# Kernel tuning notes

Measured on AMD Instinct MI355X. Metric: run time of the kernel, lower is better.

The kernel has to match this reference:

```python
import jax, jax.numpy as jnp
import numpy as np

EMBED_DIM = 1024
NUM_HEADS = 16
HEAD_DIM = EMBED_DIM // NUM_HEADS  # 64
QK_SCALE = 0.125  # head_dim ** -0.5, passed as qk_scale in __init__
B, LQ, LKV = 2, 2048, 2048


def setup_inputs() -> dict:
    key = jax.random.key(0)
    ks = jax.random.split(key, 7)
    std = 0.02
    return {
        "q": jax.random.normal(ks[0], (B, LQ, EMBED_DIM), dtype=jnp.float32),
        "k": jax.random.normal(ks[1], (B, LKV, EMBED_DIM), dtype=jnp.float32),
        "v": jax.random.normal(ks[2], (B, LKV, EMBED_DIM), dtype=jnp.float32),
        "Wq": jax.random.normal(ks[3], (EMBED_DIM, EMBED_DIM), dtype=jnp.float32) * std,
        "Wk": jax.random.normal(ks[4], (EMBED_DIM, EMBED_DIM), dtype=jnp.float32) * std,
        "Wv": jax.random.normal(ks[5], (EMBED_DIM, EMBED_DIM), dtype=jnp.float32) * std,
        "Wo": jax.random.normal(ks[6], (EMBED_DIM, EMBED_DIM), dtype=jnp.float32) * std,
    }


def _split_heads(x):
    # rearrange 'b l (c n) -> b n l c' with n = num_heads (heads are the INNER sub-dim)
    b, l, _ = x.shape
    return x.reshape(b, l, HEAD_DIM, NUM_HEADS).transpose(0, 3, 1, 2)  # (b, n, l, c)


def reference(q, k, v, Wq, Wk, Wv, Wo):
    b = q.shape[0]
    qh = _split_heads(q @ Wq)  # (b, n, lq, c)
    kh = _split_heads(k @ Wk)  # (b, n, lkv, c)
    vh = _split_heads(v @ Wv)  # (b, n, lkv, c)
    # attn = (q * qk_scale) @ k^T / sqrt(batch)
    scores = jnp.einsum('bnqc,bnkc->bnqk', qh * QK_SCALE, kh)
    scores = scores / jnp.sqrt(jnp.float32(b))
    attn = jax.nn.softmax(scores, axis=-1)
    out = jnp.einsum('bnqk,bnkc->bnqc', attn, vh)  # (b, n, lq, c)
    # merge heads back with the inverse of the (c n) split: b n l c -> b l (c n)
    out = out.transpose(0, 2, 3, 1).reshape(b, -1, HEAD_DIM * NUM_HEADS)
    return out @ Wo  # output projection (b, lq, embed_dim)
```

## Files before the change

### kernel.cpp

```cpp
#include <hip/hip_runtime.h>
#include <hip/hip_bf16.h>


typedef __attribute__((ext_vector_type(8))) short short8;
typedef __attribute__((ext_vector_type(4))) float f32x4;
typedef __attribute__((ext_vector_type(16))) float f32x16;
typedef __hip_bfloat16 bf16;

#define GLD16(g, l) __builtin_amdgcn_global_load_lds( \
    (const __attribute__((address_space(1))) void*)(g), \
    (__attribute__((address_space(3))) void*)(l), 16, 0, 0)

#define VMCNT(n) do { asm volatile("s_waitcnt vmcnt(" #n ")" ::: "memory"); \
                      __builtin_amdgcn_sched_barrier(0); } while (0)
#define BAR() do { __builtin_amdgcn_sched_barrier(0); __builtin_amdgcn_s_barrier(); \
                   __builtin_amdgcn_sched_barrier(0); } while (0)

__device__ __forceinline__ f32x4 mfma16(short8 a, short8 b, f32x4 c) {
  return __builtin_amdgcn_mfma_f32_16x16x32_bf16(a, b, c, 0, 0, 0);
}
__device__ __forceinline__ f32x16 mfma32(short8 a, short8 b, f32x16 c) {
  return __builtin_amdgcn_mfma_f32_32x32x16_bf16(a, b, c, 0, 0, 0);
}

union B8 { bf16 h[8]; int4 v; };
union B4 { bf16 h[4]; int2 v; };

#define QK_SCALE_TOT 0.08838834764831845f
#define SC2f (QK_SCALE_TOT * 1.4426950408889634f)

__device__ __forceinline__ float fexp2(float x) {
#if __has_builtin(__builtin_amdgcn_exp2f)
  return __builtin_amdgcn_exp2f(x);
#else
  return exp2f(x);
#endif
}

__device__ __forceinline__ int cvtpk(float lo, float hi_) {
  int r;
  asm("v_cvt_pk_bf16_f32 %0, %1, %2" : "=v"(r) : "v"(lo), "v"(hi_));
  return r;
}

#define ZV16 {0.f,0.f,0.f,0.f,0.f,0.f,0.f,0.f,0.f,0.f,0.f,0.f,0.f,0.f,0.f,0.f}

__global__ __launch_bounds__(256) void cast3_kernel(
    const float* __restrict__ q, const float* __restrict__ k,
    const float* __restrict__ v, bf16* __restrict__ out)
{
  const float* src = (blockIdx.y == 0) ? q : (blockIdx.y == 1) ? k : v;
  bf16* dst = out + (size_t)blockIdx.y * (4u << 20);
  size_t i = ((size_t)blockIdx.x * 256 + threadIdx.x) * 8;
  float4 a = *(const float4*)(src + i);
  float4 b = *(const float4*)(src + i + 4);
  B8 u;
  u.h[0] = __float2bfloat16(a.x); u.h[1] = __float2bfloat16(a.y);
  u.h[2] = __float2bfloat16(a.z); u.h[3] = __float2bfloat16(a.w);
  u.h[4] = __float2bfloat16(b.x); u.h[5] = __float2bfloat16(b.y);
  u.h[6] = __float2bfloat16(b.z); u.h[7] = __float2bfloat16(b.w);
  *(int4*)(dst + i) = u.v;
}

__global__ __launch_bounds__(256) void wtrans_kernel(
    const float* __restrict__ Wq, const float* __restrict__ Wk,
    const float* __restrict__ Wv, const float* __restrict__ Wo,
    bf16* __restrict__ dstbase)
{
  __shared__ bf16 ld[64][68];
  const int z = blockIdx.z;
  const float* src = (z == 0) ? Wq : (z == 1) ? Wk : (z == 2) ? Wv : Wo;
  bf16* dst = dstbase + (size_t)z * (1u << 20);
  const int k0 = blockIdx.x * 64, n0 = blockIdx.y * 64;
  const int t = threadIdx.x;
  const bool perm = (z == 3);
#pragma unroll
  for (int it = 0; it < 4; ++it) {
    int kk = it * 16 + (t >> 4);
    int K = k0 + kk;
    int j = perm ? ((K & 63) * 16 + (K >> 6)) : K;
    float4 vv = *(const float4*)(src + (size_t)j * 1024 + n0 + (t & 15) * 4);
    int c = (t & 15) * 4;
    ld[c + 0][kk] = __float2bfloat16(vv.x);
    ld[c + 1][kk] = __float2bfloat16(vv.y);
    ld[c + 2][kk] = __float2bfloat16(vv.z);
    ld[c + 3][kk] = __float2bfloat16(vv.w);
  }
  __syncthreads();
#pragma unroll
  for (int it = 0; it < 2; ++it) {
    int rr = it * 32 + (t >> 3), cc = (t & 7) * 8;
    B8 u;
#pragma unroll
    for (int e = 0; e < 8; ++e) u.h[e] = ld[rr][cc + e];
    *(int4*)(dst + (size_t)(n0 + rr) * 1024 + k0 + cc) = u.v;
  }
}

template<int FINAL>
__global__ __launch_bounds__(512, 2) void gemm8_kernel(
    const bf16* __restrict__ Abase, const bf16* __restrict__ WTbase,
    bf16* __restrict__ Qh, bf16* __restrict__ Kh, bf16* __restrict__ VhT,
    float* __restrict__ Cout)
{
  __shared__ bf16 lA[2][2][128 * 64];
  __shared__ bf16 lB[2][2][128 * 64];
  const int t = threadIdx.x, lane = t & 63, w = t >> 6;
  const int wr = w >> 2, wc = w & 3;
  const int l15 = lane & 15, l16 = lane >> 4;
  const int rswE = ((l15 >> 2) & 1) << 4;
  const int tN = blockIdx.x * 256, tM = blockIdx.y * 256;
  const int z = FINAL ? 0 : blockIdx.z;
  const bf16* A  = Abase  + (size_t)z * (4u << 20);
  const bf16* BT = WTbase + (size_t)z * (1u << 20);

  int oj[2], srj[2], scj[2];
#pragma unroll
  for (int j = 0; j < 2; ++j) {
    int o = (w * 2 + j) * 1024 + lane * 16;
    int lg = o ^ (((o >> 9) & 1) << 5);
    oj[j] = o >> 1;
    srj[j] = lg >> 7;
    scj[j] = (lg & 127) >> 1;
  }
  size_t aRow[2][2], bRow[2][2];
#pragma unroll
  for (int h = 0; h < 2; ++h)
#pragma unroll
    for (int j = 0; j < 2; ++j) {
      int r = tM + h * 128 + srj[j];
      if (FINAL)
        aRow[h][j] = ((size_t)(r >> 11) * 16 * 2048 + (r & 2047)) * 64 + scj[j];
      else
        aRow[h][j] = (size_t)r * 1024 + scj[j];
      bRow[h][j] = (size_t)(tN + h * 128 + srj[j]) * 1024 + scj[j];
    }
  const size_t aK = FINAL ? (size_t)(2048 * 64) : 64;

  auto stageA_ = [&](int buf, int h, int kt) {
    GLD16(A + aRow[h][0] + (size_t)kt * aK, &lA[buf][h][oj[0]]);
    GLD16(A + aRow[h][1] + (size_t)kt * aK, &lA[buf][h][oj[1]]);
  };
  auto stageB_ = [&](int buf, int h, int kt) {
    GLD16(BT + bRow[h][0] + (size_t)kt * 64, &lB[buf][h][oj[0]]);
    GLD16(BT + bRow[h][1] + (size_t)kt * 64, &lB[buf][h][oj[1]]);
  };
  auto readA = [&](int buf, int m, int kk) -> short8 {
    return *(const short8*)&lA[buf][wr]
        [(m * 16 + l15) * 64 + ((kk * 32 + l16 * 8) ^ rswE)];
  };
  auto readB = [&](int buf, int n, int kk) -> short8 {
    return *(const short8*)&lB[buf][wc >> 1]
        [((wc & 1) * 64 + n * 16 + l15) * 64 + ((kk * 32 + l16 * 8) ^ rswE)];
  };

  f32x4 acc[8][4];
#pragma unroll
  for (int m = 0; m < 8; ++m)
#pragma unroll
    for (int n = 0; n < 4; ++n) acc[m][n] = {0.f, 0.f, 0.f, 0.f};

  stageB_(0, 0, 0); stageB_(0, 1, 0);
  stageA_(0, 0, 0); stageA_(0, 1, 0);
  stageB_(1, 0, 1); stageB_(1, 1, 1);
  VMCNT(4);
  BAR();

  const int NIT = 8;
  for (int i = 0; i < NIT; ++i) {
    const bool more = (i + 1 < NIT);
    const int k0 = 2 * i;
    short8 bfr[4][2];
#pragma unroll
    for (int q = 0; q < 4; ++q) {
      if (q == 0) {
#pragma unroll
        for (int n = 0; n < 4; ++n)
#pragma unroll
          for (int kk = 0; kk < 2; ++kk) bfr[n][kk] = readB(0, n, kk);
      }
      short8 af[2][2];
#pragma unroll
      for (int mm = 0; mm < 2; ++mm)
#pragma unroll
        for (int kk = 0; kk < 2; ++kk) af[mm][kk] = readA(0, 2 * q + mm, kk);
      if (q == 0) stageA_(1, 0, k0 + 1);
      else if (q == 1) stageA_(1, 1, k0 + 1);
      else if (q == 2) { if (more) stageB_(0, 0, k0 + 2); }
      else             { if (more) stageB_(0, 1, k0 + 2); }
      BAR();
      __builtin_amdgcn_s_setprio(1);
#pragma unroll
      for (int mm = 0; mm < 2; ++mm)
#pragma unroll
        for (int n = 0; n < 4; ++n)
#pragma unroll
          for (int kk = 0; kk < 2; ++kk)
            acc[2 * q + mm][n] = mfma16(af[mm][kk], bfr[n][kk], acc[2 * q + mm][n]);
      __builtin_amdgcn_s_setprio(0);
      if (q == 3) { if (more) { VMCNT(4); } else { VMCNT(0); } }
      BAR();
    }
#pragma unroll
    for (int q = 0; q < 4; ++q) {
      if (q == 0) {
#pragma unroll
        for (int n = 0; n < 4; ++n)
#pragma unroll
          for (int kk = 0; kk < 2; ++kk) bfr[n][kk] = readB(1, n, kk);
      }
      short8 af[2][2];
#pragma unroll
      for (int mm = 0; mm < 2; ++mm)
#pragma unroll
        for (int kk = 0; kk < 2; ++kk) af[mm][kk] = readA(1, 2 * q + mm, kk);
      if (more) {
        if (q == 0) stageA_(0, 0, k0 + 2);
        else if (q == 1) stageA_(0, 1, k0 + 2);
        else if (q == 2) stageB_(1, 0, k0 + 3);
        else stageB_(1, 1, k0 + 3);
      }
      BAR();
      __builtin_amdgcn_s_setprio(1);
#pragma unroll
      for (int mm = 0; mm < 2; ++mm)
#pragma unroll
        for (int n = 0; n < 4; ++n)
#pragma unroll
          for (int kk = 0; kk < 2; ++kk)
            acc[2 * q + mm][n] = mfma16(af[mm][kk], bfr[n][kk], acc[2 * q + mm][n]);
      __builtin_amdgcn_s_setprio(0);
      if (q == 3 && more) VMCNT(4);
      BAR();
    }
  }

#pragma unroll
  for (int m = 0; m < 8; ++m) {
#pragma unroll
    for (int n = 0; n < 4; ++n) {
      int col = tN + wc * 64 + n * 16 + l15;
      int rbase = tM + wr * 128 + m * 16 + l16 * 4;
      if (FINAL) {
#pragma unroll
        for (int j = 0; j < 4; ++j)
          Cout[(size_t)(rbase + j) * 1024 + col] = acc[m][n][j];
      } else if (z == 2) {
        int nh = col & 15, c = col >> 4;
        int b = rbase >> 11, l0 = rbase & 2047;
        B4 u;
#pragma unroll
        for (int j = 0; j < 4; ++j) u.h[j] = __float2bfloat16(acc[m][n][j]);
        *(int2*)&VhT[((size_t)(b * 16 + nh) * 64 + c) * 2048 + l0] = u.v;
      } else {
        bf16* dst = z ? Kh : Qh;
        int nh = col & 15, c = col >> 4;
#pragma unroll
        for (int j = 0; j < 4; ++j) {
          int row = rbase + j;
          dst[((size_t)((row >> 11) * 16 + nh) * 2048 + (row & 2047)) * 64 + c] =
              __float2bfloat16(acc[m][n][j]);
        }
      }
    }
  }
}

__global__ __launch_bounds__(256) void attn_kernel(
    const bf16* __restrict__ Qh, const bf16* __restrict__ Kh,
    const bf16* __restrict__ VhT, bf16* __restrict__ Oh)
{
  __shared__ bf16 Kt[2][64 * 64];
  __shared__ bf16 Vt[2][64 * 64];
  const int t = threadIdx.x, lane = t & 63, w = t >> 6;
  const int l31 = lane & 31, hi = lane >> 5;
  const int bh = blockIdx.y;
  const int q0 = blockIdx.x * 128 + w * 32;
  const size_t baseQK = (size_t)bh * (2048 * 64);
  const size_t baseV  = (size_t)bh * (64 * 2048);

  short8 qf[4];
#pragma unroll
  for (int kc = 0; kc < 4; ++kc)
    qf[kc] = *(const short8*)&Qh[baseQK + (size_t)(q0 + l31) * 64 + kc * 16 + hi * 8];

  const int r0 = t >> 3, g0 = t & 7;
  const int sg = (g0 ^ (r0 & 7)) * 8;
  const bf16* ksrc0 = Kh  + baseQK + (size_t)r0 * 64 + sg;
  const bf16* ksrc1 = Kh  + baseQK + (size_t)(r0 + 32) * 64 + sg;
  const bf16* vsrc0 = VhT + baseV  + (size_t)r0 * 2048 + sg;
  const bf16* vsrc1 = VhT + baseV  + (size_t)(r0 + 32) * 2048 + sg;

  auto stage = [&](int buf, int ti) {
    GLD16(ksrc0 + (size_t)ti * 4096, &Kt[buf][t * 8]);
    GLD16(ksrc1 + (size_t)ti * 4096, &Kt[buf][2048 + t * 8]);
    GLD16(vsrc0 + ti * 64,           &Vt[buf][t * 8]);
    GLD16(vsrc1 + ti * 64,           &Vt[buf][2048 + t * 8]);
  };

  f32x16 o0 = ZV16, o1 = ZV16;
  float m = -1e30f, l = 0.f;
  const int swz = (l31 & 7);

  stage(0, 0);
  for (int ti = 0; ti < 32; ++ti) {
    const int buf = ti & 1;
    __syncthreads();
    if (ti < 31) stage(buf ^ 1, ti + 1);

    f32x16 s0 = ZV16, s1 = ZV16;
    __builtin_amdgcn_s_setprio(1);
#pragma unroll
    for (int kc = 0; kc < 4; ++kc) {
      const int gr = ((kc * 2 + hi) ^ swz) * 8;
      short8 kf0 = *(const short8*)&Kt[buf][l31 * 64 + gr];
      short8 kf1 = *(const short8*)&Kt[buf][(32 + l31) * 64 + gr];
      s0 = mfma32(kf0, qf[kc], s0);
      s1 = mfma32(kf1, qf[kc], s1);
    }
    __builtin_amdgcn_s_setprio(0);

    float tm8[8];
#pragma unroll
    for (int i2 = 0; i2 < 8; ++i2)
      tm8[i2] = fmaxf(fmaxf(s0[i2], s0[i2 + 8]), fmaxf(s1[i2], s1[i2 + 8]));
    float pm = fmaxf(fmaxf(fmaxf(tm8[0], tm8[1]), fmaxf(tm8[2], tm8[3])),
                     fmaxf(fmaxf(tm8[4], tm8[5]), fmaxf(tm8[6], tm8[7])));
    pm = fmaxf(pm, __shfl_xor(pm, 32));
    float mn = fmaxf(m, pm);
    float corr = fexp2((m - mn) * SC2f);
    m = mn;
    float nb = -mn * SC2f;
#pragma unroll
    for (int r = 0; r < 16; ++r) {
      s0[r] = fexp2(s0[r] * SC2f + nb);
      s1[r] = fexp2(s1[r] * SC2f + nb);
    }
    float ts8[8];
#pragma unroll
    for (int i2 = 0; i2 < 8; ++i2)
      ts8[i2] = (s0[i2] + s0[i2 + 8]) + (s1[i2] + s1[i2 + 8]);
    float rs = ((ts8[0] + ts8[1]) + (ts8[2] + ts8[3])) +
               ((ts8[4] + ts8[5]) + (ts8[6] + ts8[7]));
    rs += __shfl_xor(rs, 32);
    l = l * corr + rs;
#pragma unroll
    for (int r = 0; r < 16; ++r) { o0[r] *= corr; o1[r] *= corr; }

    short8 pf[4];
    {
      union U { int i[4]; short8 s8; } fr[4];
      int wds[16];
#pragma unroll
      for (int j = 0; j < 8; ++j) wds[j]     = cvtpk(s0[2 * j], s0[2 * j + 1]);
#pragma unroll
      for (int j = 0; j < 8; ++j) wds[8 + j] = cvtpk(s1[2 * j], s1[2 * j + 1]);
#pragma unroll
      for (int fb = 0; fb < 4; ++fb) {
        int a0 = wds[fb * 4 + 0], a1 = wds[fb * 4 + 1];
        int a2 = wds[fb * 4 + 2], a3 = wds[fb * 4 + 3];
#if __has_builtin(__builtin_amdgcn_permlane32_swap)
        auto s02 = __builtin_amdgcn_permlane32_swap(a0, a2, false, false);
        auto s13 = __builtin_amdgcn_permlane32_swap(a1, a3, false, false);
        fr[fb].i[0] = s02[0]; fr[fb].i[1] = s13[0];
        fr[fb].i[2] = s02[1]; fr[fb].i[3] = s13[1];
#else
        int x0 = __shfl_xor(a0, 32), x2 = __shfl_xor(a2, 32);
        int x1 = __shfl_xor(a1, 32), x3 = __shfl_xor(a3, 32);
        fr[fb].i[0] = hi ? x2 : a0; fr[fb].i[1] = hi ? x3 : a1;
        fr[fb].i[2] = hi ? a2 : x0; fr[fb].i[3] = hi ? a3 : x1;
#endif
        pf[fb] = fr[fb].s8;
      }
    }

    __builtin_amdgcn_s_setprio(1);
#pragma unroll
    for (int kc = 0; kc < 4; ++kc) {
      const int gr = ((kc * 2 + hi) ^ swz) * 8;
      short8 vf0 = *(const short8*)&Vt[buf][l31 * 64 + gr];
      short8 vf1 = *(const short8*)&Vt[buf][(32 + l31) * 64 + gr];
      o0 = mfma32(vf0, pf[kc], o0);
      o1 = mfma32(vf1, pf[kc], o1);
    }
    __builtin_amdgcn_s_setprio(0);
  }

  float rl = 1.0f / l;
  bf16* orow = Oh + baseQK + (size_t)(q0 + l31) * 64;
#pragma unroll
  for (int rq = 0; rq < 4; ++rq) {
    B4 u0, u1;
#pragma unroll
    for (int j = 0; j < 4; ++j) {
      u0.h[j] = __float2bfloat16(o0[rq * 4 + j] * rl);
      u1.h[j] = __float2bfloat16(o1[rq * 4 + j] * rl);
    }
    int dbase = rq * 8 + hi * 4;
    *(int2*)&orow[dbase]      = u0.v;
    *(int2*)&orow[32 + dbase] = u1.v;
  }
}

extern "C" void kernel_launch(void* const* d_in, const int* in_sizes, int n_in,
                              void* d_out, int out_size, void* d_ws, size_t ws_size,
                              hipStream_t stream) {
  const float* q  = (const float*)d_in[0];
  const float* k  = (const float*)d_in[1];
  const float* v  = (const float*)d_in[2];
  const float* Wq = (const float*)d_in[3];
  const float* Wk = (const float*)d_in[4];
  const float* Wv = (const float*)d_in[5];
  const float* Wo = (const float*)d_in[6];
  char* ws = (char*)d_ws;
  const size_t MB = 1u << 20;
  bf16* xb  = (bf16*)(ws);
  bf16* WT  = (bf16*)(ws + 24 * MB);
  bf16* Qh  = (bf16*)(ws + 32 * MB);
  bf16* Kh  = (bf16*)(ws + 40 * MB);
  bf16* VhT = (bf16*)(ws + 48 * MB);
  bf16* Oh  = (bf16*)(ws);

  cast3_kernel<<<dim3(2048, 3), 256, 0, stream>>>(q, k, v, xb);
  wtrans_kernel<<<dim3(16, 16, 4), 256, 0, stream>>>(Wq, Wk, Wv, Wo, WT);
  gemm8_kernel<0><<<dim3(4, 16, 3), 512, 0, stream>>>(xb, WT, Qh, Kh, VhT, nullptr);
  attn_kernel<<<dim3(16, 32), 256, 0, stream>>>(Qh, Kh, VhT, Oh);
  gemm8_kernel<1><<<dim3(4, 16), 512, 0, stream>>>(Oh, WT + 3 * (1u << 20), Qh, Kh, VhT,
                                                   (float*)d_out);
}
```

Baseline: 300.9 us.

## Add dedicated small-tile output-projection GEMM and swizzle block order in QKV GEMM

Replaces the templated 256x256-tile output projection (only 64 blocks) with a new 128x64-tile kernel using a triple-buffered LDS pipeline and XOR swizzling, launched as 512 blocks so more CUs are busy. The QKV GEMM gets a block-index remap that groups tiles for better L2 reuse. Its sched_barrier fences are removed and an explicit lgkmcnt(0) wait is added before the MFMAs, giving the compiler more freedom to schedule around the barriers. The risks are lower per-block reuse in the small-tile kernel and a changed instruction schedule in the main GEMM.

```diff
diff --git a/kernel.cpp b/kernel.cpp
--- a/kernel.cpp
+++ b/kernel.cpp
@@ -11,10 +11,8 @@
     (const __attribute__((address_space(1))) void*)(g), \
     (__attribute__((address_space(3))) void*)(l), 16, 0, 0)
 
-#define VMCNT(n) do { asm volatile("s_waitcnt vmcnt(" #n ")" ::: "memory"); \
-                      __builtin_amdgcn_sched_barrier(0); } while (0)
-#define BAR() do { __builtin_amdgcn_sched_barrier(0); __builtin_amdgcn_s_barrier(); \
-                   __builtin_amdgcn_sched_barrier(0); } while (0)
+#define VMCNT(n) asm volatile("s_waitcnt vmcnt(" #n ")" ::: "memory")
+#define LGKM0()  asm volatile("s_waitcnt lgkmcnt(0)" ::: "memory")
 
 __device__ __forceinline__ f32x4 mfma16(short8 a, short8 b, f32x4 c) {
   return __builtin_amdgcn_mfma_f32_16x16x32_bf16(a, b, c, 0, 0, 0);
@@ -97,11 +95,9 @@
   }
 }
 
-template<int FINAL>
 __global__ __launch_bounds__(512, 2) void gemm8_kernel(
     const bf16* __restrict__ Abase, const bf16* __restrict__ WTbase,
-    bf16* __restrict__ Qh, bf16* __restrict__ Kh, bf16* __restrict__ VhT,
-    float* __restrict__ Cout)
+    bf16* __restrict__ Qh, bf16* __restrict__ Kh, bf16* __restrict__ VhT)
 {
   __shared__ bf16 lA[2][2][128 * 64];
   __shared__ bf16 lB[2][2][128 * 64];
@@ -109,8 +105,10 @@
   const int wr = w >> 2, wc = w & 3;
   const int l15 = lane & 15, l16 = lane >> 4;
   const int rswE = ((l15 >> 2) & 1) << 4;
-  const int tN = blockIdx.x * 256, tM = blockIdx.y * 256;
-  const int z = FINAL ? 0 : blockIdx.z;
+  const int nblk = blockIdx.x + 4 * blockIdx.y;
+  const int sblk = (nblk & 7) * 8 + (nblk >> 3);
+  const int tN = (sblk & 3) * 256, tM = (sblk >> 2) * 256;
+  const int z = blockIdx.z;
   const bf16* A  = Abase  + (size_t)z * (4u << 20);
   const bf16* BT = WTbase + (size_t)z * (1u << 20);
 
@@ -128,18 +126,13 @@
   for (int h = 0; h < 2; ++h)
 #pragma unroll
     for (int j = 0; j < 2; ++j) {
-      int r = tM + h * 128 + srj[j];
-      if (FINAL)
-        aRow[h][j] = ((size_t)(r >> 11) * 16 * 2048 + (r & 2047)) * 64 + scj[j];
-      else
-        aRow[h][j] = (size_t)r * 1024 + scj[j];
+      aRow[h][j] = (size_t)(tM + h * 128 + srj[j]) * 1024 + scj[j];
       bRow[h][j] = (size_t)(tN + h * 128 + srj[j]) * 1024 + scj[j];
     }
-  const size_t aK = FINAL ? (size_t)(2048 * 64) : 64;
 
   auto stageA_ = [&](int buf, int h, int kt) {
-    GLD16(A + aRow[h][0] + (size_t)kt * aK, &lA[buf][h][oj[0]]);
-    GLD16(A + aRow[h][1] + (size_t)kt * aK, &lA[buf][h][oj[1]]);
+    GLD16(A + aRow[h][0] + (size_t)kt * 64, &lA[buf][h][oj[0]]);
+    GLD16(A + aRow[h][1] + (size_t)kt * 64, &lA[buf][h][oj[1]]);
   };
   auto stageB_ = [&](int buf, int h, int kt) {
     GLD16(BT + bRow[h][0] + (size_t)kt * 64, &lB[buf][h][oj[0]]);
@@ -164,7 +157,7 @@
   stageA_(0, 0, 0); stageA_(0, 1, 0);
   stageB_(1, 0, 1); stageB_(1, 1, 1);
   VMCNT(4);
-  BAR();
+  __builtin_amdgcn_s_barrier();
 
   const int NIT = 8;
   for (int i = 0; i < NIT; ++i) {
@@ -188,7 +181,8 @@
       else if (q == 1) stageA_(1, 1, k0 + 1);
       else if (q == 2) { if (more) stageB_(0, 0, k0 + 2); }
       else             { if (more) stageB_(0, 1, k0 + 2); }
-      BAR();
+      __builtin_amdgcn_s_barrier();
+      LGKM0();
       __builtin_amdgcn_s_setprio(1);
 #pragma unroll
       for (int mm = 0; mm < 2; ++mm)
@@ -199,7 +193,7 @@
             acc[2 * q + mm][n] = mfma16(af[mm][kk], bfr[n][kk], acc[2 * q + mm][n]);
       __builtin_amdgcn_s_setprio(0);
       if (q == 3) { if (more) { VMCNT(4); } else { VMCNT(0); } }
-      BAR();
+      __builtin_amdgcn_s_barrier();
     }
 #pragma unroll
     for (int q = 0; q < 4; ++q) {
@@ -220,7 +214,8 @@
         else if (q == 2) stageB_(1, 0, k0 + 3);
         else stageB_(1, 1, k0 + 3);
       }
-      BAR();
+      __builtin_amdgcn_s_barrier();
+      LGKM0();
       __builtin_amdgcn_s_setprio(1);
 #pragma unroll
       for (int mm = 0; mm < 2; ++mm)
@@ -231,7 +226,7 @@
             acc[2 * q + mm][n] = mfma16(af[mm][kk], bfr[n][kk], acc[2 * q + mm][n]);
       __builtin_amdgcn_s_setprio(0);
       if (q == 3 && more) VMCNT(4);
-      BAR();
+      __builtin_amdgcn_s_barrier();
     }
   }
 
@@ -241,11 +236,7 @@
     for (int n = 0; n < 4; ++n) {
       int col = tN + wc * 64 + n * 16 + l15;
       int rbase = tM + wr * 128 + m * 16 + l16 * 4;
-      if (FINAL) {
-#pragma unroll
-        for (int j = 0; j < 4; ++j)
-          Cout[(size_t)(rbase + j) * 1024 + col] = acc[m][n][j];
-      } else if (z == 2) {
+      if (z == 2) {
         int nh = col & 15, c = col >> 4;
         int b = rbase >> 11, l0 = rbase & 2047;
         B4 u;
@@ -264,6 +255,93 @@
       }
     }
   }
+}
+
+__global__ __launch_bounds__(256) void gemmo_kernel(
+    const bf16* __restrict__ Oh, const bf16* __restrict__ WoT,
+    float* __restrict__ Cout)
+{
+  __shared__ bf16 lA[3][128 * 64];
+  __shared__ bf16 lB[3][64 * 64];
+  const int t = threadIdx.x, lane = t & 63, w = t >> 6;
+  const int wr = w >> 1, wc = w & 1;
+  const int l15 = lane & 15, l16 = lane >> 4;
+  const int gsw = l15 & 7;
+  const int nblk = blockIdx.x + 16 * blockIdx.y;
+  const int sblk = (nblk & 7) * 64 + (nblk >> 3);
+  const int tN = (sblk & 15) * 64, tM = (sblk >> 4) * 128;
+
+  const int ca = (((t & 7) ^ ((t >> 3) & 7)) * 8);
+  size_t aoff[4], boff[2];
+#pragma unroll
+  for (int i = 0; i < 4; ++i) {
+    int rg = tM + i * 32 + (t >> 3);
+    aoff[i] = ((size_t)(rg >> 11) * 16 * 2048 + (rg & 2047)) * 64 + ca;
+  }
+#pragma unroll
+  for (int i = 0; i < 2; ++i)
+    boff[i] = (size_t)(tN + i * 32 + (t >> 3)) * 1024 + ca;
+
+  auto stage = [&](int b, int kt) {
+#pragma unroll
+    for (int i = 0; i < 4; ++i)
+      GLD16(Oh + aoff[i] + (size_t)kt * (2048 * 64), &lA[b][(i * 256 + t) * 8]);
+#pragma unroll
+    for (int i = 0; i < 2; ++i)
+      GLD16(WoT + boff[i] + kt * 64, &lB[b][(i * 256 + t) * 8]);
+  };
+
+  f32x4 acc[4][2];
+#pragma unroll
+  for (int m = 0; m < 4; ++m)
+#pragma unroll
+    for (int n = 0; n < 2; ++n) acc[m][n] = {0.f, 0.f, 0.f, 0.f};
+
+  stage(0, 0); stage(1, 1);
+  VMCNT(6);
+  __builtin_amdgcn_s_barrier();
+
+  int bR = 0, bS = 2;
+  for (int kt = 0; kt < 16; ++kt) {
+    if (kt < 14) stage(bS, kt + 2);
+    short8 a_[4][2], b_[2][2];
+#pragma unroll
+    for (int m = 0; m < 4; ++m)
+#pragma unroll
+      for (int kk = 0; kk < 2; ++kk) {
+        int row = wr * 64 + m * 16 + l15;
+        a_[m][kk] = *(const short8*)&lA[bR][row * 64 + (((kk * 4 + l16) ^ gsw) * 8)];
+      }
+#pragma unroll
+    for (int n = 0; n < 2; ++n)
+#pragma unroll
+      for (int kk = 0; kk < 2; ++kk) {
+        int row = wc * 32 + n * 16 + l15;
+        b_[n][kk] = *(const short8*)&lB[bR][row * 64 + (((kk * 4 + l16) ^ gsw) * 8)];
+      }
+#pragma unroll
+    for (int kk = 0; kk < 2; ++kk)
+#pragma unroll
+      for (int m = 0; m < 4; ++m)
+#pragma unroll
+        for (int n = 0; n < 2; ++n)
+          acc[m][n] = mfma16(a_[m][kk], b_[n][kk], acc[m][n]);
+    if (kt < 14) { VMCNT(6); } else { VMCNT(0); }
+    __builtin_amdgcn_s_barrier();
+    bR = (bR == 2) ? 0 : bR + 1;
+    bS = (bS == 2) ? 0 : bS + 1;
+  }
+
+#pragma unroll
+  for (int m = 0; m < 4; ++m)
+#pragma unroll
+    for (int n = 0; n < 2; ++n) {
+      int col = tN + wc * 32 + n * 16 + l15;
+      int rbase = tM + wr * 64 + m * 16 + l16 * 4;
+#pragma unroll
+      for (int j = 0; j < 4; ++j)
+        Cout[(size_t)(rbase + j) * 1024 + col] = acc[m][n][j];
+    }
 }
 
 __global__ __launch_bounds__(256) void attn_kernel(
@@ -423,8 +501,8 @@
 
   cast3_kernel<<<dim3(2048, 3), 256, 0, stream>>>(q, k, v, xb);
   wtrans_kernel<<<dim3(16, 16, 4), 256, 0, stream>>>(Wq, Wk, Wv, Wo, WT);
-  gemm8_kernel<0><<<dim3(4, 16, 3), 512, 0, stream>>>(xb, WT, Qh, Kh, VhT, nullptr);
+  gemm8_kernel<<<dim3(4, 16, 3), 512, 0, stream>>>(xb, WT, Qh, Kh, VhT);
   attn_kernel<<<dim3(16, 32), 256, 0, stream>>>(Qh, Kh, VhT, Oh);
-  gemm8_kernel<1><<<dim3(4, 16), 512, 0, stream>>>(Oh, WT + 3 * (1u << 20), Qh, Kh, VhT,
-                                                   (float*)d_out);
-}
+  gemmo_kernel<<<dim3(16, 32), 256, 0, stream>>>(Oh, WT + 3 * (1u << 20),
+                                                 (float*)d_out);
+}
```

After: 276.1 us. -8.2%, faster.
